# Kernel optimization log

Hardware: AMD Instinct MI355X
Metric: run time of the kernel (lower is better)

The kernel has to match this reference:

```python
import jax, jax.numpy as jnp
import numpy as np

DIM = 1024
N_HEADS = 16
HEAD_DIM = DIM // N_HEADS


def setup_inputs() -> dict:
    key = jax.random.key(0)
    ks = jax.random.split(key, 5)
    scale = 1.0 / np.sqrt(DIM)
    x = jax.random.normal(ks[0], (2, 2048, DIM), dtype=jnp.float32)
    W_qkv = jax.random.normal(ks[1], (DIM, 3 * DIM), dtype=jnp.float32) * scale
    b_qkv = jax.random.normal(ks[2], (3 * DIM,), dtype=jnp.float32) * 0.01
    W_proj = jax.random.normal(ks[3], (DIM, DIM), dtype=jnp.float32) * scale
    b_proj = jax.random.normal(ks[4], (DIM,), dtype=jnp.float32) * 0.01
    return {"x": x, "W_qkv": W_qkv, "b_qkv": b_qkv, "W_proj": W_proj, "b_proj": b_proj}


def reference(x, W_qkv, b_qkv, W_proj, b_proj):
    B, T, C = x.shape
    qkv = x @ W_qkv + b_qkv  # [B,T,3C]
    q, k, v = jnp.split(qkv, 3, axis=2)
    # [B,T,C] -> [B,H,T,Dh]
    def heads(y):
        return y.reshape(B, T, N_HEADS, HEAD_DIM).transpose(0, 2, 1, 3)
    q, k, v = heads(q), heads(k), heads(v)
    inv_sqrt_dh = 1.0 / jnp.sqrt(jnp.asarray(HEAD_DIM, dtype=x.dtype))
    attn = jnp.einsum('bhqd,bhkd->bhqk', q, k) * inv_sqrt_dh
    attn = jax.nn.softmax(attn, axis=-1)
    out = jnp.einsum('bhqk,bhkd->bhqd', attn, v)
    out = out.transpose(0, 2, 1, 3).reshape(B, T, C)
    return out @ W_proj + b_proj
```

## Files before the change

### kernel.cpp

```cpp
#include <hip/hip_runtime.h>
#include <hip/hip_bf16.h>
#include <math.h>

using bf16 = __hip_bfloat16;

typedef __bf16 bf16x8 __attribute__((ext_vector_type(8)));
typedef __bf16 bf16x4 __attribute__((ext_vector_type(4)));
typedef float  f32x4  __attribute__((ext_vector_type(4)));
typedef float  f32x16 __attribute__((ext_vector_type(16)));

constexpr int Bb = 2;
constexpr int Ts = 2048;
constexpr int Cc = 1024;
constexpr int Hh = 16;
constexpr int Dh = 64;
constexpr int Mm = Bb * Ts;
constexpr int Nqkv = 3 * Cc;
constexpr int BHTD = Bb * Hh * Ts * Dh;

__device__ __forceinline__
void gll16(const __bf16* g, __bf16* l)
{
    __builtin_amdgcn_global_load_lds(
        (const __attribute__((address_space(1))) unsigned int*)g,
        (__attribute__((address_space(3))) unsigned int*)l,
        16, 0, 0);
}

__global__ __launch_bounds__(256)
void prep_all(const float* __restrict__ x, __bf16* __restrict__ Xb,
              const float* __restrict__ Wq, __bf16* __restrict__ Wqt,
              const float* __restrict__ Wp, __bf16* __restrict__ Wpt)
{
    __shared__ __bf16 tl[64][72];
    const int bid = blockIdx.x;
    const int t = threadIdx.x;

    if (bid < 4096) {
        int i = (bid * 256 + t) * 4;
        float4 v = *(const float4*)(x + i);
        bf16x4 o = { (__bf16)v.x, (__bf16)v.y, (__bf16)v.z, (__bf16)v.w };
        *(bf16x4*)(Xb + i) = o;
        return;
    }
    const float* W; __bf16* Wt; int cols, bx, by;
    if (bid < 4096 + 768) {
        W = Wq; Wt = Wqt; cols = Nqkv;
        bx = (bid - 4096) % 48; by = (bid - 4096) / 48;
    } else {
        W = Wp; Wt = Wpt; cols = Cc;
        bx = (bid - 4864) % 16; by = (bid - 4864) / 16;
    }
    const int c0 = bx * 64;
    const int r0 = by * 64;
    #pragma unroll
    for (int i = 0; i < 4; i++) {
        int e = t + 256 * i;
        int r = e >> 4, c4 = (e & 15) * 4;
        float4 v = *(const float4*)(W + (r0 + r) * cols + c0 + c4);
        bf16x4 o = { (__bf16)v.x, (__bf16)v.y, (__bf16)v.z, (__bf16)v.w };
        *(bf16x4*)&tl[r][c4] = o;
    }
    __syncthreads();
    #pragma unroll
    for (int i = 0; i < 4; i++) {
        int e = t + 256 * i;
        int n = e >> 4, k4 = (e & 15) * 4;
        bf16x4 o = { tl[k4][n], tl[k4 + 1][n], tl[k4 + 2][n], tl[k4 + 3][n] };
        *(bf16x4*)(Wt + (c0 + n) * 1024 + r0 + k4) = o;
    }
}

template<int BM>
__device__ __forceinline__
void gemm_core64(__bf16 (*Al)[64], __bf16 (*Bl)[64],
                 const __bf16* __restrict__ A, const __bf16* __restrict__ Bt,
                 int m0, int n0, int wm, int wn, int quad, int l16, int t,
                 f32x4 (&acc)[4][4])
{
    constexpr int MT = BM / 32;
    const int wave = t >> 6;
    const int lane = t & 63;
    const int srow = lane >> 3;
    const int scol = ((lane & 7) ^ srow) * 8;

    const __bf16* Ag = A  + (size_t)(m0 + wave * (BM / 4) + srow) * 1024 + scol;
    const __bf16* Bg = Bt + (size_t)(n0 + wave * 32 + srow) * 1024 + scol;

    const int swz = (l16 & 7) << 4;

    for (int k0 = 0; k0 < 1024; k0 += 64) {
        #pragma unroll
        for (int g = 0; g < BM / 32; g++)
            gll16(Ag + k0 + (size_t)g * 8 * 1024, &Al[wave * (BM / 4) + g * 8][0]);
        #pragma unroll
        for (int g = 0; g < 4; g++)
            gll16(Bg + k0 + (size_t)g * 8 * 1024, &Bl[wave * 32 + g * 8][0]);
        __syncthreads();
        #pragma unroll
        for (int ks = 0; ks < 2; ks++) {
            const int cb = (ks * 64 + quad * 16) ^ swz;
            bf16x8 af[MT], bfr[4];
            #pragma unroll
            for (int mt = 0; mt < MT; mt++)
                af[mt] = *(const bf16x8*)((const char*)&Al[wm * (BM / 2) + mt * 16 + l16][0] + cb);
            #pragma unroll
            for (int nt = 0; nt < 4; nt++)
                bfr[nt] = *(const bf16x8*)((const char*)&Bl[wn * 64 + nt * 16 + l16][0] + cb);
            #pragma unroll
            for (int mt = 0; mt < MT; mt++)
                #pragma unroll
                for (int nt = 0; nt < 4; nt++)
                    acc[mt][nt] = __builtin_amdgcn_mfma_f32_16x16x32_bf16(
                        af[mt], bfr[nt], acc[mt][nt], 0, 0, 0);
        }
        __syncthreads();
    }
}

__global__ __launch_bounds__(256)
void qkv_mfma(const __bf16* __restrict__ A, const __bf16* __restrict__ Bt,
              const float* __restrict__ bias, __bf16* __restrict__ qkv)
{
    __shared__ __align__(16) char smem[36864];
    __bf16 (*Al)[64] = (__bf16(*)[64])smem;
    __bf16 (*Bl)[64] = (__bf16(*)[64])(smem + 16384);
    typedef __bf16 (*ebuf_p)[64][72];
    ebuf_p ebuf = (ebuf_p)smem;

    const int t    = threadIdx.x;
    const int wave = t >> 6;
    const int lane = t & 63;
    const int quad = lane >> 4;
    const int l16  = lane & 15;
    const int wm   = wave >> 1, wn = wave & 1;
    const int bid  = blockIdx.x;
    const int swb  = (bid & 7) * 96 + (bid >> 3);
    const int n0 = (swb % 24) * 128;
    const int m0 = (swb / 24) * 128;

    f32x4 acc[4][4];
    #pragma unroll
    for (int i = 0; i < 4; i++)
        #pragma unroll
        for (int j = 0; j < 4; j++)
            acc[i][j] = f32x4{0.f, 0.f, 0.f, 0.f};

    gemm_core64<128>(Al, Bl, A, Bt, m0, n0, wm, wn, quad, l16, t, acc);

    const int nw0 = n0 + wn * 64;
    const int which = nw0 >> 10;
    const int h = (nw0 & 1023) >> 6;

    if (which == 2) {
        #pragma unroll
        for (int nt = 0; nt < 4; nt++) {
            int d = nt * 16 + l16;
            float bs = bias[nw0 + nt * 16 + l16];
            #pragma unroll
            for (int mt = 0; mt < 4; mt++) {
                int m = m0 + wm * 64 + mt * 16 + quad * 4;
                int b = m >> 11;
                int tt = m & 2047;
                bf16x4 o = { (__bf16)(acc[mt][nt][0] + bs),
                             (__bf16)(acc[mt][nt][1] + bs),
                             (__bf16)(acc[mt][nt][2] + bs),
                             (__bf16)(acc[mt][nt][3] + bs) };
                *(bf16x4*)&qkv[2 * (size_t)BHTD +
                               (((size_t)(b * 16 + h) * 64 + d) * 2048 + tt)] = o;
            }
        }
    } else {
        #pragma unroll
        for (int nt = 0; nt < 4; nt++) {
            float bs = bias[nw0 + nt * 16 + l16];
            #pragma unroll
            for (int mt = 0; mt < 4; mt++)
                #pragma unroll
                for (int r = 0; r < 4; r++)
                    ebuf[wave][mt * 16 + quad * 4 + r][nt * 16 + l16] =
                        (__bf16)(acc[mt][nt][r] + bs);
        }
        int m = m0 + wm * 64 + lane;
        int b = m >> 11;
        int tt = m & 2047;
        __bf16* dst = &qkv[which * (size_t)BHTD +
                           (((size_t)(b * 16 + h) * 2048 + tt) * 64)];
        #pragma unroll
        for (int c = 0; c < 8; c++)
            *(bf16x8*)(dst + c * 8) = *(const bf16x8*)&ebuf[wave][lane][c * 8];
    }
}

__global__ __launch_bounds__(256)
void proj_mfma(const __bf16* __restrict__ A, const __bf16* __restrict__ Bt,
               const float* __restrict__ bias, float* __restrict__ out)
{
    __shared__ __bf16 Al[64][64];
    __shared__ __bf16 Bl[128][64];

    const int t    = threadIdx.x;
    const int wave = t >> 6;
    const int lane = t & 63;
    const int quad = lane >> 4;
    const int l16  = lane & 15;
    const int wm   = wave >> 1, wn = wave & 1;
    const int bid  = blockIdx.x;
    const int swb  = (bid & 7) * 64 + (bid >> 3);
    const int n0 = (swb & 7) * 128;
    const int m0 = (swb >> 3) * 64;

    f32x4 acc[4][4];
    #pragma unroll
    for (int i = 0; i < 4; i++)
        #pragma unroll
        for (int j = 0; j < 4; j++)
            acc[i][j] = f32x4{0.f, 0.f, 0.f, 0.f};

    gemm_core64<64>(Al, Bl, A, Bt, m0, n0, wm, wn, quad, l16, t, acc);

    #pragma unroll
    for (int nt = 0; nt < 4; nt++) {
        int n = n0 + wn * 64 + nt * 16 + l16;
        float bs = bias[n];
        #pragma unroll
        for (int mt = 0; mt < 2; mt++) {
            #pragma unroll
            for (int r = 0; r < 4; r++) {
                int m = m0 + wm * 32 + mt * 16 + quad * 4 + r;
                out[m * 1024 + n] = acc[mt][nt][r] + bs;
            }
        }
    }
}

__global__ __launch_bounds__(512, 2)
void attn_mfma(const __bf16* __restrict__ Q, const __bf16* __restrict__ K,
               const __bf16* __restrict__ VT, __bf16* __restrict__ O)
{
    __shared__ __bf16 sK[2][3][64 * 64];
    __shared__ __bf16 sV[2][3][64 * 64];
    __shared__ float  slsum[4][2][64];

    const int t    = threadIdx.x;
    const int wave = t >> 6;
    const int lane = t & 63;
    const int qg   = wave & 3;
    const int kh   = wave >> 2;
    const int c    = lane & 31;
    const int hi   = lane >> 5;
    const int hx   = hi * 16;
    const int sw   = (c & 7) << 4;

    const int blk = blockIdx.x;
    const int bh  = blk & 31;
    const int qc  = blk >> 5;
    const int q0  = qc * 256 + qg * 64;

    const __bf16* Qp = Q  + ((size_t)bh * Ts + q0) * Dh;
    const __bf16* Kp = K  + (size_t)bh * Ts * Dh;
    const __bf16* Vp = VT + (size_t)bh * Dh * Ts;

    const float qscale = 0.125f * 1.44269504088896f;
    bf16x8 qf[2][4];
    #pragma unroll
    for (int qs = 0; qs < 2; qs++)
        #pragma unroll
        for (int ds = 0; ds < 4; ds++) {
            bf16x8 v = *(const bf16x8*)(Qp + (qs * 32 + c) * Dh + ds * 16 + hi * 8);
            #pragma unroll
            for (int i = 0; i < 8; i++) v[i] = (__bf16)(qscale * (float)v[i]);
            qf[qs][ds] = v;
        }

    f32x16 accO[2][2];
    #pragma unroll
    for (int qs = 0; qs < 2; qs++)
        #pragma unroll
        for (int dt = 0; dt < 2; dt++)
            #pragma unroll
            for (int i = 0; i < 16; i++) accO[qs][dt][i] = 0.f;
    float lsum[2] = {0.f, 0.f};

    const f32x16 z16 = {0.f, 0.f, 0.f, 0.f, 0.f, 0.f, 0.f, 0.f,
                        0.f, 0.f, 0.f, 0.f, 0.f, 0.f, 0.f, 0.f};

    const int r0 = qg * 8 + (lane >> 3);
    const int s8 = ((lane & 7) ^ (r0 & 7)) * 8;
    const __bf16* kg0 = Kp + (size_t)(kh * 1024 + r0) * Dh + s8;
    const __bf16* kg1 = kg0 + 32 * Dh;
    const __bf16* vg0 = Vp + (size_t)r0 * Ts + kh * 1024 + s8;
    const __bf16* vg1 = vg0 + (size_t)32 * Ts;

    gll16(kg0, &sK[kh][0][qg * 512]);
    gll16(kg1, &sK[kh][0][2048 + qg * 512]);
    gll16(vg0, &sV[kh][0][qg * 512]);
    gll16(vg1, &sV[kh][0][2048 + qg * 512]);

    for (int j = 0; j < 16; j++) {
        const int p = j % 3;
        if (j < 15) {
            const int pn = (j + 1) % 3;
            gll16(kg0 + (j + 1) * 4096, &sK[kh][pn][qg * 512]);
            gll16(kg1 + (j + 1) * 4096, &sK[kh][pn][2048 + qg * 512]);
            gll16(vg0 + (j + 1) * 64,   &sV[kh][pn][qg * 512]);
            gll16(vg1 + (j + 1) * 64,   &sV[kh][pn][2048 + qg * 512]);
            asm volatile("s_waitcnt vmcnt(4)" ::: "memory");
        } else {
            asm volatile("s_waitcnt vmcnt(0)" ::: "memory");
        }
        __builtin_amdgcn_s_barrier();
        __builtin_amdgcn_sched_barrier(0);

        const char* kb = (const char*)&sK[kh][p][0];
        const char* vb = (const char*)&sV[kh][p][0];

        bf16x8 kf[2][4];
        #pragma unroll
        for (int kt = 0; kt < 2; kt++) {
            const char* rbase = kb + (kt * 32 + c) * 128;
            #pragma unroll
            for (int ds = 0; ds < 4; ds++)
                kf[kt][ds] = *(const bf16x8*)(rbase + ((ds * 32 + hx) ^ sw));
        }

        f32x16 st[2][2];
        __builtin_amdgcn_s_setprio(1);
        #pragma unroll
        for (int kt = 0; kt < 2; kt++)
            #pragma unroll
            for (int qs = 0; qs < 2; qs++)
                st[qs][kt] = __builtin_amdgcn_mfma_f32_32x32x16_bf16(
                    kf[kt][0], qf[qs][0], z16, 0, 0, 0);
        #pragma unroll
        for (int ds = 1; ds < 4; ds++)
            #pragma unroll
            for (int kt = 0; kt < 2; kt++)
                #pragma unroll
                for (int qs = 0; qs < 2; qs++)
                    st[qs][kt] = __builtin_amdgcn_mfma_f32_32x32x16_bf16(
                        kf[kt][ds], qf[qs][ds], st[qs][kt], 0, 0, 0);
        __builtin_amdgcn_s_setprio(0);

        bf16x8 pa[2][4];
        #pragma unroll
        for (int qs = 0; qs < 2; qs++) {
            unsigned pk[2][8];
            #pragma unroll
            for (int kt = 0; kt < 2; kt++) {
                float sum0 = 0.f, sum1 = 0.f;
                #pragma unroll
                for (int r = 0; r < 16; r++) {
                    float pv = __builtin_amdgcn_exp2f(st[qs][kt][r]);
                    st[qs][kt][r] = pv;
                    if (r & 1) sum1 += pv; else sum0 += pv;
                }
                lsum[qs] += sum0 + sum1;
                #pragma unroll
                for (int r2 = 0; r2 < 8; r2++) {
                    unsigned d;
                    asm("v_cvt_pk_bf16_f32 %0, %1, %2"
                        : "=v"(d)
                        : "v"(st[qs][kt][2 * r2]), "v"(st[qs][kt][2 * r2 + 1]));
                    pk[kt][r2] = d;
                }
            }
            #pragma unroll
            for (int s = 0; s < 4; s++) {
                const int kt = s >> 1, r4 = (s & 1) * 4;
                unsigned x0 = pk[kt][r4 + 0], y0 = pk[kt][r4 + 2];
                unsigned x1 = pk[kt][r4 + 1], y1 = pk[kt][r4 + 3];
                asm("v_permlane32_swap_b32 %0, %1" : "+v"(x0), "+v"(y0));
                asm("v_permlane32_swap_b32 %0, %1" : "+v"(x1), "+v"(y1));
                union { unsigned u[4]; bf16x8 b; } pu;
                pu.u[0] = x0; pu.u[1] = x1; pu.u[2] = y0; pu.u[3] = y1;
                pa[qs][s] = pu.b;
            }
        }

        __builtin_amdgcn_s_setprio(1);
        #pragma unroll
        for (int s = 0; s < 4; s++)
            #pragma unroll
            for (int dt = 0; dt < 2; dt++) {
                bf16x8 vf = *(const bf16x8*)(vb + (dt * 32 + c) * 128 +
                                             ((s * 32 + hx) ^ sw));
                #pragma unroll
                for (int qs = 0; qs < 2; qs++)
                    accO[qs][dt] = __builtin_amdgcn_mfma_f32_32x32x16_bf16(
                        pa[qs][s], vf, accO[qs][dt], 0, 0, 0);
            }
        __builtin_amdgcn_s_setprio(0);
    }

    __syncthreads();

    float* pb = (qg < 2) ? (float*)&sK[0][0][0] + qg * 4096
                         : (float*)&sV[0][0][0] + (qg - 2) * 4096;
    if (kh == 1) {
        #pragma unroll
        for (int qs = 0; qs < 2; qs++) {
            #pragma unroll
            for (int dt = 0; dt < 2; dt++)
                #pragma unroll
                for (int r = 0; r < 16; r++)
                    pb[((qs * 2 + dt) << 10) + (r << 6) + lane] = accO[qs][dt][r];
            slsum[qg][qs][lane] = lsum[qs];
        }
    }
    __syncthreads();
    if (kh == 0) {
        #pragma unroll
        for (int qs = 0; qs < 2; qs++) {
            #pragma unroll
            for (int dt = 0; dt < 2; dt++)
                #pragma unroll
                for (int r = 0; r < 16; r++)
                    accO[qs][dt][r] += pb[((qs * 2 + dt) << 10) + (r << 6) + lane];
            lsum[qs] += slsum[qg][qs][lane];
        }

        const int b = bh >> 4, h = bh & 15;
        #pragma unroll
        for (int qs = 0; qs < 2; qs++) {
            float l = lsum[qs] + __shfl_xor(lsum[qs], 32);
            float linv = 1.f / l;
            #pragma unroll
            for (int r = 0; r < 16; r++) {
                const int qrow = (r & 3) + 8 * (r >> 2) + 4 * hi;
                float inv = __shfl(linv, qrow);
                __bf16* Op = O + ((size_t)(b * Ts + q0 + qs * 32 + qrow)) * Cc +
                             h * 64 + c;
                Op[0]  = (__bf16)(accO[qs][0][r] * inv);
                Op[32] = (__bf16)(accO[qs][1][r] * inv);
            }
        }
    }
}

extern "C" void kernel_launch(void* const* d_in, const int* in_sizes, int n_in,
                              void* d_out, int out_size, void* d_ws, size_t ws_size,
                              hipStream_t stream)
{
    (void)in_sizes; (void)n_in; (void)out_size; (void)ws_size;
    const float* x     = (const float*)d_in[0];
    const float* Wqkv  = (const float*)d_in[1];
    const float* bqkv  = (const float*)d_in[2];
    const float* Wproj = (const float*)d_in[3];
    const float* bproj = (const float*)d_in[4];
    float* out = (float*)d_out;

    __bf16* ws   = (__bf16*)d_ws;
    __bf16* Qw   = ws;
    __bf16* XbAO = ws + 3 * (size_t)BHTD;
    __bf16* Wqt  = XbAO + (size_t)Mm * Cc;
    __bf16* Wpt  = Wqt + (size_t)Nqkv * Cc;

    prep_all<<<dim3(5120), 256, 0, stream>>>(x, XbAO, Wqkv, Wqt, Wproj, Wpt);
    qkv_mfma<<<dim3(768), 256, 0, stream>>>(XbAO, Wqt, bqkv, Qw);
    attn_mfma<<<dim3(256), 512, 0, stream>>>(
        Qw, Qw + BHTD, Qw + 2 * (size_t)BHTD, XbAO);
    proj_mfma<<<dim3(512), 256, 0, stream>>>(XbAO, Wpt, bproj, out);
}
```

Baseline: 181.5 us.

## Triple-buffer GEMM K-loop with async LDS loads and single barrier per step

Replaces the single-buffered 64-wide K loop in the QKV and projection GEMMs with a triple-buffered 32-wide K pipeline. The next tile's global-to-LDS loads are issued before computing the current one, with explicit vmcnt waits and one barrier per step. The goal is to hide global load latency behind MFMA work and drop the second barrier per iteration. In exchange it uses more LDS, runs twice as many loop steps, and depends on hand-counted vmcnt values being correct.

```diff
diff --git a/kernel.cpp b/kernel.cpp
--- a/kernel.cpp
+++ b/kernel.cpp
@@ -73,58 +73,80 @@
 
 template<int BM>
 __device__ __forceinline__
-void gemm_core64(__bf16 (*Al)[64], __bf16 (*Bl)[64],
-                 const __bf16* __restrict__ A, const __bf16* __restrict__ Bt,
-                 int m0, int n0, int wm, int wn, int quad, int l16, int t,
-                 f32x4 (&acc)[4][4])
-{
-    constexpr int MT = BM / 32;
+void gemm_core_tb(__bf16* sbuf,
+                  const __bf16* __restrict__ A, const __bf16* __restrict__ Bt,
+                  int m0, int n0, int wm, int wn, int quad, int l16, int t,
+                  f32x4 (&acc)[4][4])
+{
+    constexpr int MT   = BM / 32;
+    constexpr int AG   = BM / 64;
+    constexpr int STEP = (BM + 128) * 32;
+
     const int wave = t >> 6;
     const int lane = t & 63;
-    const int srow = lane >> 3;
-    const int scol = ((lane & 7) ^ srow) * 8;
+    const int srow = lane >> 2;
+    const int scol = ((lane & 3) ^ (srow & 3)) * 8;
 
     const __bf16* Ag = A  + (size_t)(m0 + wave * (BM / 4) + srow) * 1024 + scol;
     const __bf16* Bg = Bt + (size_t)(n0 + wave * 32 + srow) * 1024 + scol;
 
-    const int swz = (l16 & 7) << 4;
-
-    for (int k0 = 0; k0 < 1024; k0 += 64) {
-        #pragma unroll
-        for (int g = 0; g < BM / 32; g++)
-            gll16(Ag + k0 + (size_t)g * 8 * 1024, &Al[wave * (BM / 4) + g * 8][0]);
-        #pragma unroll
-        for (int g = 0; g < 4; g++)
-            gll16(Bg + k0 + (size_t)g * 8 * 1024, &Bl[wave * 32 + g * 8][0]);
-        __syncthreads();
-        #pragma unroll
-        for (int ks = 0; ks < 2; ks++) {
-            const int cb = (ks * 64 + quad * 16) ^ swz;
-            bf16x8 af[MT], bfr[4];
-            #pragma unroll
-            for (int mt = 0; mt < MT; mt++)
-                af[mt] = *(const bf16x8*)((const char*)&Al[wm * (BM / 2) + mt * 16 + l16][0] + cb);
+    {
+        __bf16* Alp = sbuf;
+        __bf16* Blp = sbuf + BM * 32;
+        #pragma unroll
+        for (int g = 0; g < AG; g++)
+            gll16(Ag + (size_t)g * 16 * 1024, &Alp[(wave * (BM / 4) + g * 16) * 32]);
+        gll16(Bg,                      &Blp[(wave * 32) * 32]);
+        gll16(Bg + (size_t)16 * 1024,  &Blp[(wave * 32 + 16) * 32]);
+    }
+
+    const int cb = (quad ^ (l16 & 3)) * 16;
+
+    for (int j = 0; j < 32; j++) {
+        const int p = j % 3;
+        if (j < 31) {
+            const int pn = (j + 1) % 3;
+            const int k1 = (j + 1) * 32;
+            __bf16* Alp = sbuf + pn * STEP;
+            __bf16* Blp = Alp + BM * 32;
+            #pragma unroll
+            for (int g = 0; g < AG; g++)
+                gll16(Ag + k1 + (size_t)g * 16 * 1024,
+                      &Alp[(wave * (BM / 4) + g * 16) * 32]);
+            gll16(Bg + k1,                     &Blp[(wave * 32) * 32]);
+            gll16(Bg + k1 + (size_t)16 * 1024, &Blp[(wave * 32 + 16) * 32]);
+            if constexpr (AG == 2) asm volatile("s_waitcnt vmcnt(4)" ::: "memory");
+            else                   asm volatile("s_waitcnt vmcnt(3)" ::: "memory");
+        } else {
+            asm volatile("s_waitcnt vmcnt(0)" ::: "memory");
+        }
+        __builtin_amdgcn_s_barrier();
+        __builtin_amdgcn_sched_barrier(0);
+
+        const char* Alp = (const char*)(sbuf + p * STEP);
+        const char* Blp = (const char*)(sbuf + p * STEP + BM * 32);
+        bf16x8 af[MT], bfr[4];
+        #pragma unroll
+        for (int mt = 0; mt < MT; mt++)
+            af[mt] = *(const bf16x8*)(Alp + (wm * (BM / 2) + mt * 16 + l16) * 64 + cb);
+        #pragma unroll
+        for (int nt = 0; nt < 4; nt++)
+            bfr[nt] = *(const bf16x8*)(Blp + (wn * 64 + nt * 16 + l16) * 64 + cb);
+        #pragma unroll
+        for (int mt = 0; mt < MT; mt++)
             #pragma unroll
             for (int nt = 0; nt < 4; nt++)
-                bfr[nt] = *(const bf16x8*)((const char*)&Bl[wn * 64 + nt * 16 + l16][0] + cb);
-            #pragma unroll
-            for (int mt = 0; mt < MT; mt++)
-                #pragma unroll
-                for (int nt = 0; nt < 4; nt++)
-                    acc[mt][nt] = __builtin_amdgcn_mfma_f32_16x16x32_bf16(
-                        af[mt], bfr[nt], acc[mt][nt], 0, 0, 0);
-        }
-        __syncthreads();
-    }
+                acc[mt][nt] = __builtin_amdgcn_mfma_f32_16x16x32_bf16(
+                    af[mt], bfr[nt], acc[mt][nt], 0, 0, 0);
+    }
+    __syncthreads();
 }
 
 __global__ __launch_bounds__(256)
 void qkv_mfma(const __bf16* __restrict__ A, const __bf16* __restrict__ Bt,
               const float* __restrict__ bias, __bf16* __restrict__ qkv)
 {
-    __shared__ __align__(16) char smem[36864];
-    __bf16 (*Al)[64] = (__bf16(*)[64])smem;
-    __bf16 (*Bl)[64] = (__bf16(*)[64])(smem + 16384);
+    __shared__ __align__(16) __bf16 smem[3 * (128 + 128) * 32];
     typedef __bf16 (*ebuf_p)[64][72];
     ebuf_p ebuf = (ebuf_p)smem;
 
@@ -146,7 +168,7 @@
         for (int j = 0; j < 4; j++)
             acc[i][j] = f32x4{0.f, 0.f, 0.f, 0.f};
 
-    gemm_core64<128>(Al, Bl, A, Bt, m0, n0, wm, wn, quad, l16, t, acc);
+    gemm_core_tb<128>(smem, A, Bt, m0, n0, wm, wn, quad, l16, t, acc);
 
     const int nw0 = n0 + wn * 64;
     const int which = nw0 >> 10;
@@ -196,8 +218,7 @@
 void proj_mfma(const __bf16* __restrict__ A, const __bf16* __restrict__ Bt,
                const float* __restrict__ bias, float* __restrict__ out)
 {
-    __shared__ __bf16 Al[64][64];
-    __shared__ __bf16 Bl[128][64];
+    __shared__ __align__(16) __bf16 smem[3 * (64 + 128) * 32];
 
     const int t    = threadIdx.x;
     const int wave = t >> 6;
@@ -217,7 +238,7 @@
         for (int j = 0; j < 4; j++)
             acc[i][j] = f32x4{0.f, 0.f, 0.f, 0.f};
 
-    gemm_core64<64>(Al, Bl, A, Bt, m0, n0, wm, wn, quad, l16, t, acc);
+    gemm_core_tb<64>(smem, A, Bt, m0, n0, wm, wn, quad, l16, t, acc);
 
     #pragma unroll
     for (int nt = 0; nt < 4; nt++) {
```

New measurement: 182.3 us. Within noise of the previous version (+0.4%).
